# Optimization experiments

Measured on AMD Instinct MI355X. Metric: run time of the kernel, lower is better.

## Reference

```python
import jax, jax.numpy as jnp
import numpy as np
import math

HEAD_DIM = 128
NUM_HEADS = 16
ROPE_BASE = 10000.0


def _rope(x, st_pos):
    # x: [B, S, H, hd], interleaved even/odd rotation as in the torch module
    S, hd = x.shape[1], x.shape[3]
    theta = 1.0 / (ROPE_BASE ** (jnp.arange(0, hd, 2, dtype=jnp.float32) / hd))  # [hd/2]
    pos = jnp.arange(st_pos, st_pos + S, dtype=jnp.float32)[:, None]             # [S,1]
    ang = pos * theta                                                            # [S, hd/2]
    sin = jnp.sin(ang)[None, :, None, :]
    cos = jnp.cos(ang)[None, :, None, :]
    xe, xo = x[..., 0::2], x[..., 1::2]
    re = xe * cos - xo * sin
    ro = xe * sin + xo * cos
    # re-interleave: stack pairs then flatten last two dims
    return jnp.stack([re, ro], axis=-1).reshape(x.shape)


def setup_inputs() -> dict:
    key = jax.random.key(0)
    ks = jax.random.split(key, 6)
    B, S, D = 4, 2048, 2048
    scale = 1.0 / math.sqrt(D)
    x = jax.random.normal(ks[0], (B, S, D), dtype=jnp.float32)
    # causal additive mask (prefill)
    mask = jnp.where(jnp.tril(jnp.ones((S, S), dtype=bool)), 0.0, -1e9).astype(jnp.float32)
    Wq = jax.random.normal(ks[1], (D, NUM_HEADS * HEAD_DIM), dtype=jnp.float32) * scale
    Wk = jax.random.normal(ks[2], (D, NUM_HEADS * HEAD_DIM), dtype=jnp.float32) * scale
    Wv = jax.random.normal(ks[3], (D, NUM_HEADS * HEAD_DIM), dtype=jnp.float32) * scale
    Wo = jax.random.normal(ks[4], (NUM_HEADS * HEAD_DIM, D), dtype=jnp.float32) * scale
    return {"x": x, "mask": mask, "Wq": Wq, "Wk": Wk, "Wv": Wv, "Wo": Wo, "st_pos": 0}


def reference(x, mask, Wq, Wk, Wv, Wo, st_pos):
    B, S, D = x.shape
    H, hd = NUM_HEADS, HEAD_DIM
    q = (x @ Wq).reshape(B, S, H, hd)
    k = (x @ Wk).reshape(B, S, H, hd)
    v = (x @ Wv).reshape(B, S, H, hd)
    q = _rope(q, st_pos)
    k = _rope(k, st_pos)
    # st_pos=0 prefill: cache slice == current k, v; n_rep == 1 (n_kv_heads=num_heads)
    scores = jnp.einsum('bqhd,bkhd->bhqk', q, k) / math.sqrt(hd)
    if mask is not None:
        scores = scores + mask
    attn = jax.nn.softmax(scores, axis=-1)
    a = jnp.einsum('bhqk,bkhd->bqhd', attn, v).reshape(B, S, H * hd)
    return a @ Wo
```

## Files before the change

kernel.cpp:

```cpp
#include <hip/hip_runtime.h>
#include <hip/hip_fp16.h>

typedef _Float16 f16;
typedef __attribute__((ext_vector_type(2))) _Float16 f16x2;
typedef __attribute__((ext_vector_type(4))) _Float16 f16x4v;
typedef __attribute__((ext_vector_type(8))) _Float16 f16x8;
typedef __attribute__((ext_vector_type(4))) float f32x4;
typedef __attribute__((ext_vector_type(4))) int i32x4;

#define DEV __device__ __forceinline__

static constexpr int S_ = 2048;
static constexpr int D_ = 2048;
static constexpr int H_ = 16;
static constexpr int HD_ = 128;
static constexpr int B_ = 4;
static constexpr int QKV_ST = 6144;

typedef const __attribute__((address_space(1))) void* gptr_t;
typedef __attribute__((address_space(3))) void* lptr_t;

DEV void gl_lds16(const void* gsrc, void* lds) {
  __builtin_amdgcn_global_load_lds((gptr_t)gsrc, (lptr_t)lds, 16, 0, 0);
}

DEV int cvt_pk_i32(float a, float b) {
  return __builtin_bit_cast(int, __builtin_amdgcn_cvt_pkrtz(a, b));
}

__global__ __launch_bounds__(256) void cvt_f32_to_f16(const float* __restrict__ in,
                                                      f16* __restrict__ out, long n) {
  long i0 = ((long)blockIdx.x * 256 + threadIdx.x) * 4;
  long stride = (long)gridDim.x * 256 * 4;
  for (long i = i0; i < n; i += stride) {
    float4 v = *(const float4*)(in + i);
    f16x4v o;
    o[0] = (f16)v.x; o[1] = (f16)v.y; o[2] = (f16)v.z; o[3] = (f16)v.w;
    *(f16x4v*)(out + i) = o;
  }
}

__global__ __launch_bounds__(256) void wtrans4(const float* __restrict__ W0, const float* __restrict__ W1,
                                               const float* __restrict__ W2, const float* __restrict__ W3,
                                               f16* __restrict__ Wt) {
  __shared__ float tile[32][33];
  int wi = blockIdx.y;
  const float* W = wi == 0 ? W0 : wi == 1 ? W1 : wi == 2 ? W2 : W3;
  f16* dst = Wt + (size_t)wi * D_ * D_;
  int bx = blockIdx.x & 63, by = blockIdx.x >> 6;
  int r0 = by << 5, c0 = bx << 5;
  int tx = threadIdx.x & 31, ty = threadIdx.x >> 5;
#pragma unroll
  for (int i = 0; i < 4; i++) {
    int r = ty + i * 8;
    tile[r][tx] = W[(size_t)(r0 + r) * D_ + c0 + tx];
  }
  __syncthreads();
#pragma unroll
  for (int i = 0; i < 4; i++) {
    int r = ty + i * 8;
    dst[(size_t)(c0 + r) * D_ + r0 + tx] = (f16)tile[tx][r];
  }
}

DEV f16x8 lds_frag(const f16* half, int row, int s, int lg) {
  int byte = row * 128 + s * 64 + lg * 16;
  byte ^= (row & 4) << 3;
  return *(const f16x8*)((const char*)half + byte);
}

template <typename CT>
__global__ __launch_bounds__(512, 2) void gemm8(const f16* __restrict__ A, const f16* __restrict__ Bt,
                                                CT* __restrict__ C, int M, int N, int K,
                                                int lda, int ldc) {
  __shared__ alignas(16) f16 As[2][2][128 * 64];
  __shared__ alignas(16) f16 Bs[2][2][128 * 64];
  int nbx = N >> 8;
  int nwg = (M >> 8) * nbx;
  int bid = blockIdx.x;
  int wg = (bid & 7) * (nwg >> 3) + (bid >> 3);
  int bx = wg % nbx, by = wg / nbx;
  int tid = threadIdx.x, w = tid >> 6, l = tid & 63;
  int wm = w >> 2, wn = w & 3, lg = l >> 4, ln = l & 15;
  int nt = K >> 6;
  const f16* Ab = A + (size_t)(by * 256) * lda;
  const f16* Bb = Bt + (size_t)(bx * 256) * K;

  auto stageA = [&](const f16* src0, int kt, f16* dst) {
#pragma unroll
    for (int j = 0; j < 2; j++) {
      int c = j * 8 + w;
      int row = c * 8 + (l >> 3);
      int scol = ((l & 7) * 8) ^ ((row & 4) << 2);
      gl_lds16(src0 + (size_t)row * lda + kt * 64 + scol, (char*)dst + c * 1024);
    }
  };
  auto stageB = [&](const f16* src0, int kt, f16* dst) {
#pragma unroll
    for (int j = 0; j < 2; j++) {
      int c = j * 8 + w;
      int row = c * 8 + (l >> 3);
      int scol = ((l & 7) * 8) ^ ((row & 4) << 2);
      gl_lds16(src0 + (size_t)row * K + kt * 64 + scol, (char*)dst + c * 1024);
    }
  };

  f32x4 acc[8][4] = {};

  stageA(Ab, 0, As[0][0]);
  stageA(Ab + (size_t)128 * lda, 0, As[0][1]);
  stageB(Bb, 0, Bs[0][0]);
  stageB(Bb + (size_t)128 * K, 0, Bs[0][1]);
  if (nt > 1) {
    stageB(Bb, 1, Bs[1][0]);
    stageB(Bb + (size_t)128 * K, 1, Bs[1][1]);
  }

  for (int t = 0; t < nt; t++) {
    if (t + 2 < nt) asm volatile("s_waitcnt vmcnt(4)" ::: "memory");
    else            asm volatile("s_waitcnt vmcnt(0)" ::: "memory");
    __builtin_amdgcn_s_barrier();
    asm volatile("" ::: "memory");
    const f16* Ah = As[t & 1][wm];
    const f16* Bh = Bs[t & 1][wn >> 1];
    int br0 = (wn & 1) * 64;
    f16x8 a[4], b0[4], b1[4];
#pragma unroll
    for (int i = 0; i < 4; i++) a[i] = lds_frag(Ah, i * 16 + ln, 0, lg);
#pragma unroll
    for (int i = 0; i < 4; i++) b0[i] = lds_frag(Bh, br0 + i * 16 + ln, 0, lg);
    if (t + 1 < nt) stageA(Ab, t + 1, As[(t + 1) & 1][0]);
    __builtin_amdgcn_s_barrier();
    asm volatile("" ::: "memory");
    __builtin_amdgcn_s_setprio(1);
#pragma unroll
    for (int mi = 0; mi < 4; mi++)
#pragma unroll
      for (int ni = 0; ni < 4; ni++)
        acc[mi][ni] = __builtin_amdgcn_mfma_f32_16x16x32_f16(a[mi], b0[ni], acc[mi][ni], 0, 0, 0);
    __builtin_amdgcn_s_setprio(0);
    __builtin_amdgcn_s_barrier();
    asm volatile("" ::: "memory");
#pragma unroll
    for (int i = 0; i < 4; i++) a[i] = lds_frag(Ah, i * 16 + ln, 1, lg);
#pragma unroll
    for (int i = 0; i < 4; i++) b1[i] = lds_frag(Bh, br0 + i * 16 + ln, 1, lg);
    if (t + 1 < nt) stageA(Ab + (size_t)128 * lda, t + 1, As[(t + 1) & 1][1]);
    __builtin_amdgcn_s_barrier();
    asm volatile("" ::: "memory");
    __builtin_amdgcn_s_setprio(1);
#pragma unroll
    for (int mi = 0; mi < 4; mi++)
#pragma unroll
      for (int ni = 0; ni < 4; ni++)
        acc[mi][ni] = __builtin_amdgcn_mfma_f32_16x16x32_f16(a[mi], b1[ni], acc[mi][ni], 0, 0, 0);
    __builtin_amdgcn_s_setprio(0);
    __builtin_amdgcn_s_barrier();
    asm volatile("" ::: "memory");
#pragma unroll
    for (int i = 0; i < 4; i++) a[i] = lds_frag(Ah, 64 + i * 16 + ln, 0, lg);
    if (t + 2 < nt) stageB(Bb, t + 2, Bs[t & 1][0]);
    __builtin_amdgcn_s_barrier();
    asm volatile("" ::: "memory");
    __builtin_amdgcn_s_setprio(1);
#pragma unroll
    for (int mi = 0; mi < 4; mi++)
#pragma unroll
      for (int ni = 0; ni < 4; ni++)
        acc[mi + 4][ni] = __builtin_amdgcn_mfma_f32_16x16x32_f16(a[mi], b0[ni], acc[mi + 4][ni], 0, 0, 0);
    __builtin_amdgcn_s_setprio(0);
    __builtin_amdgcn_s_barrier();
    asm volatile("" ::: "memory");
#pragma unroll
    for (int i = 0; i < 4; i++) a[i] = lds_frag(Ah, 64 + i * 16 + ln, 1, lg);
    if (t + 2 < nt) stageB(Bb + (size_t)128 * K, t + 2, Bs[t & 1][1]);
    __builtin_amdgcn_s_barrier();
    asm volatile("" ::: "memory");
    __builtin_amdgcn_s_setprio(1);
#pragma unroll
    for (int mi = 0; mi < 4; mi++)
#pragma unroll
      for (int ni = 0; ni < 4; ni++)
        acc[mi + 4][ni] = __builtin_amdgcn_mfma_f32_16x16x32_f16(a[mi], b1[ni], acc[mi + 4][ni], 0, 0, 0);
    __builtin_amdgcn_s_setprio(0);
    __builtin_amdgcn_s_barrier();
    asm volatile("" ::: "memory");
  }

  int row0 = by * 256 + wm * 128;
  int col0 = bx * 256 + wn * 64;
#pragma unroll
  for (int mi = 0; mi < 8; mi++)
#pragma unroll
    for (int ni = 0; ni < 4; ni++)
#pragma unroll
      for (int r4 = 0; r4 < 4; r4++) {
        int row = row0 + mi * 16 + lg * 4 + r4;
        int col = col0 + ni * 16 + ln;
        float o = acc[mi][ni][r4];
        if constexpr (sizeof(CT) == 2) {
          float oo = __shfl_xor(o, 1);
          if (!(ln & 1)) {
            f16x2 pp; pp[0] = (f16)o; pp[1] = (f16)oo;
            *(f16x2*)(&C[(size_t)row * ldc + col]) = pp;
          }
        } else {
          C[(size_t)row * ldc + col] = o;
        }
      }
}

__global__ __launch_bounds__(256) void rope_table(float2* __restrict__ tab, const int* __restrict__ st) {
  int i = blockIdx.x * 256 + threadIdx.x;
  int s = i >> 6, j = i & 63;
  float theta = powf(10000.f, -(float)j / 64.f);
  float ang = (float)(s + st[0]) * theta;
  tab[i] = make_float2(cosf(ang), sinf(ang));
}

__global__ __launch_bounds__(256) void rope_apply_k(f16* __restrict__ QKV, const float2* __restrict__ tab,
                                                    long npairs) {
  long i0 = (long)blockIdx.x * 256 + threadIdx.x;
  long stride = (long)gridDim.x * 256;
  for (long p = i0; p < npairs; p += stride) {
    long row = p >> 10;
    int jp = (int)(p & 1023);
    int s = (int)(row & (S_ - 1));
    float2 cs = tab[s * 64 + (jp & 63)];
    f16* px = QKV + row * QKV_ST + 2048 + 2 * jp;
    f16x2 v = *(const f16x2*)px;
    float xe = (float)v[0], xo = (float)v[1];
    float re = xe * cs.x - xo * cs.y;
    float ro = xe * cs.y + xo * cs.x;
    f16x2 o; o[0] = (f16)re; o[1] = (f16)ro;
    *(f16x2*)px = o;
  }
}

__global__ __launch_bounds__(256) void vtrans2(const f16* __restrict__ QKV, f16* __restrict__ VT2) {
  __shared__ alignas(16) f16 tile[64 * 128];
  int t = blockIdx.x, bh = blockIdx.y, b = bh >> 4, h = bh & 15;
  int tid = threadIdx.x, w = tid >> 6, l = tid & 63, lg = l >> 4, ln = l & 15;
  const f16* src = QKV + (size_t)(b * S_ + t * 64) * QKV_ST + 4096 + h * HD_;
#pragma unroll
  for (int i = 0; i < 4; i++) {
    int idx = i * 256 + tid;
    int r = idx >> 4, c8 = idx & 15;
    int c8s = c8 ^ ((r >> 3) & 3);
    *(f16x8*)(&tile[r * 128 + c8s * 8]) = *(const f16x8*)(src + (size_t)r * QKV_ST + c8 * 8);
  }
  __syncthreads();
  f16* dst = VT2 + (size_t)(bh * 32 + t) * 16 * 512;
#pragma unroll
  for (int ci = 0; ci < 4; ci++) {
    int c = w * 4 + ci;
    int nj = c >> 1, kk = c & 1;
    f16x8 v;
#pragma unroll
    for (int e = 0; e < 8; e++) {
      int r = 16 * (2 * kk + (e >> 2)) + 4 * lg + (e & 3);
      int col = nj * 16 + ln;
      int c8s = (col >> 3) ^ ((r >> 3) & 3);
      v[e] = tile[r * 128 + c8s * 8 + (col & 7)];
    }
    *(f16x8*)(dst + (size_t)c * 512 + l * 8) = v;
  }
}

__global__ __launch_bounds__(512, 4) void attn(f16* __restrict__ QKV, const f16* __restrict__ VT2,
                                               const float2* __restrict__ tab) {
  __shared__ alignas(16) f16 kls[2][2][64 * 128];
  int id = blockIdx.x;
  int r8 = id & 7, j = id >> 3;
  int u = j & 7, g = j >> 3;
  int bh = r8 + (g << 3);
  int b = bh >> 4, h = bh & 15;
  int tid = threadIdx.x, w = tid >> 6, l = tid & 63, lg = l >> 4, ln = l & 15;

  const float QSCALE = 0.12751744910173355f;
  const f16* kp = QKV + (size_t)(b * S_) * QKV_ST + 2048 + h * HD_;
  const f16* vp2 = VT2 + (size_t)bh * 32 * 16 * 512;

  auto stageK = [&](int buf, int half, int kv0) {
#pragma unroll
    for (int jj = 0; jj < 2; jj++) {
      int i = jj * 8 + w;
      int byte = i * 1024 + 16 * l;
      int r = byte >> 8;
      int c = (((byte >> 4) & 15) - r) & 15;
      gl_lds16(kp + (size_t)(kv0 + r) * QKV_ST + c * 8, (char*)kls[buf][half] + i * 1024);
    }
  };

#pragma unroll 1
  for (int pi = 0; pi < 2; pi++) {
    int qsel = pi ? u : 15 - u;
    int q0 = qsel << 7;
    int qrow = q0 + w * 16 + ln;
    f16* qp = QKV + (size_t)(b * S_ + qrow) * QKV_ST + h * HD_;
    const float2* tq = tab + (size_t)qrow * 64;
    f16x8 qf[4];
#pragma unroll
    for (int kc = 0; kc < 4; kc++) {
      f16x8 q = *(const f16x8*)(qp + kc * 32 + lg * 8);
#pragma unroll
      for (int p = 0; p < 4; p++) {
        float2 cs = tq[kc * 16 + lg * 4 + p];
        float e0 = (float)q[2 * p], e1 = (float)q[2 * p + 1];
        q[2 * p] = (f16)((e0 * cs.x - e1 * cs.y) * QSCALE);
        q[2 * p + 1] = (f16)((e0 * cs.y + e1 * cs.x) * QSCALE);
      }
      qf[kc] = q;
    }

    float m = -1e30f, lsum = 0.f;
    f32x4 oacc[8] = {};

    int np = qsel + 1;
    int nt64 = 2 * qsel + 2;
    if (pi) __syncthreads();
    stageK(0, 0, 0);
    stageK(0, 1, 64);
#pragma unroll 1
    for (int p = 0; p < np; p++) {
      __syncthreads();
      if (p + 1 < np) {
        stageK((p + 1) & 1, 0, (2 * p + 2) << 6);
        stageK((p + 1) & 1, 1, (2 * p + 3) << 6);
      }
#pragma unroll 1
      for (int ii = 0; ii < 2; ii++) {
        int t = 2 * p + ii;
        int kv0 = t << 6;
        if (kv0 > q0 + w * 16 + 15) continue;
        const f16* kb = kls[p & 1][ii];
        const f16* vt = vp2 + (size_t)t * 16 * 512;

        f32x4 sf[4];
        __builtin_amdgcn_s_setprio(1);
#pragma unroll
        for (int ni = 0; ni < 4; ni++) {
          int n = ni * 16 + ln;
          f32x4 s = {0.f, 0.f, 0.f, 0.f};
#pragma unroll
          for (int kc = 0; kc < 4; kc++) {
            int mch = kc * 4 + lg;
            f16x8 kf = *(const f16x8*)(&kb[n * 128 + (((mch + n) & 15) << 3)]);
            s = __builtin_amdgcn_mfma_f32_16x16x32_f16(kf, qf[kc], s, 0, 0, 0);
          }
          sf[ni] = s;
        }
        __builtin_amdgcn_s_setprio(0);

        f16x8 vfa[8];
#pragma unroll
        for (int c = 0; c < 8; c++) vfa[c] = *(const f16x8*)(vt + c * 512 + l * 8);

        if (t >= nt64 - 2) {
#pragma unroll
          for (int ni = 0; ni < 4; ni++) {
            int kvg = kv0 + ni * 16 + lg * 4;
#pragma unroll
            for (int r4 = 0; r4 < 4; r4++)
              if (kvg + r4 > qrow) sf[ni][r4] = -1e30f;
          }
        }
        float pm = fmaxf(fmaxf(fmaxf(sf[0][0], sf[0][1]), fmaxf(sf[0][2], sf[0][3])),
                         fmaxf(fmaxf(sf[1][0], sf[1][1]), fmaxf(sf[1][2], sf[1][3])));
        pm = fmaxf(pm, fmaxf(fmaxf(fmaxf(sf[2][0], sf[2][1]), fmaxf(sf[2][2], sf[2][3])),
                             fmaxf(fmaxf(sf[3][0], sf[3][1]), fmaxf(sf[3][2], sf[3][3]))));
        pm = fmaxf(pm, __shfl_xor(pm, 16));
        pm = fmaxf(pm, __shfl_xor(pm, 32));
        float scl = 1.f;
        bool defer = __all(pm <= m + 8.f);
        if (!defer) {
          float mn = fmaxf(m, pm);
          scl = __builtin_amdgcn_exp2f(m - mn);
          m = mn;
        }
        float rsum = 0.f;
#pragma unroll
        for (int ni = 0; ni < 4; ni++)
#pragma unroll
          for (int r4 = 0; r4 < 4; r4++) {
            float pv = __builtin_amdgcn_exp2f(sf[ni][r4] - m);
            sf[ni][r4] = pv;
            rsum += pv;
          }
        lsum = lsum * scl + rsum;

        if (!defer) {
#pragma unroll
          for (int nj = 0; nj < 8; nj++)
#pragma unroll
            for (int r4 = 0; r4 < 4; r4++) oacc[nj][r4] *= scl;
        }

        f16x8 pa[2];
#pragma unroll
        for (int kk = 0; kk < 2; kk++) {
          i32x4 wv;
          wv.x = cvt_pk_i32(sf[2 * kk][0], sf[2 * kk][1]);
          wv.y = cvt_pk_i32(sf[2 * kk][2], sf[2 * kk][3]);
          wv.z = cvt_pk_i32(sf[2 * kk + 1][0], sf[2 * kk + 1][1]);
          wv.w = cvt_pk_i32(sf[2 * kk + 1][2], sf[2 * kk + 1][3]);
          pa[kk] = __builtin_bit_cast(f16x8, wv);
        }

        __builtin_amdgcn_s_setprio(1);
#pragma unroll
        for (int kk = 0; kk < 2; kk++)
#pragma unroll
          for (int nj = 0; nj < 4; nj++)
            oacc[nj] = __builtin_amdgcn_mfma_f32_16x16x32_f16(vfa[nj * 2 + kk], pa[kk], oacc[nj], 0, 0, 0);
#pragma unroll
        for (int njb = 0; njb < 2; njb++) {
          f16x8 vf[4];
#pragma unroll
          for (int jj = 0; jj < 2; jj++)
#pragma unroll
            for (int kk = 0; kk < 2; kk++)
              vf[jj * 2 + kk] = *(const f16x8*)(vt + (size_t)(((4 + njb * 2 + jj) * 2 + kk) * 512) + l * 8);
#pragma unroll
          for (int kk = 0; kk < 2; kk++)
#pragma unroll
            for (int jj = 0; jj < 2; jj++)
              oacc[4 + njb * 2 + jj] = __builtin_amdgcn_mfma_f32_16x16x32_f16(
                  vf[jj * 2 + kk], pa[kk], oacc[4 + njb * 2 + jj], 0, 0, 0);
        }
        __builtin_amdgcn_s_setprio(0);
      }
    }

    lsum += __shfl_xor(lsum, 16);
    lsum += __shfl_xor(lsum, 32);
    float inv = 1.f / lsum;
#pragma unroll
    for (int nj = 0; nj < 8; nj++) {
      f16x4v ov;
#pragma unroll
      for (int r4 = 0; r4 < 4; r4++) ov[r4] = (f16)(oacc[nj][r4] * inv);
      *(f16x4v*)(qp + nj * 16 + lg * 4) = ov;
    }
  }
}

extern "C" void kernel_launch(void* const* d_in, const int* in_sizes, int n_in,
                              void* d_out, int out_size, void* d_ws, size_t ws_size,
                              hipStream_t stream) {
  (void)in_sizes; (void)n_in; (void)out_size; (void)ws_size;
  const float* x = (const float*)d_in[0];
  const float* Wq = (const float*)d_in[2];
  const float* Wk = (const float*)d_in[3];
  const float* Wv = (const float*)d_in[4];
  const float* Wo = (const float*)d_in[5];
  const int* stp = (const int*)d_in[6];
  float* out = (float*)d_out;

  const size_t MS = (size_t)B_ * S_;
  f16* xh = (f16*)d_ws;
  f16* wqt = xh + MS * D_;
  f16* wkt = wqt + (size_t)D_ * D_;
  f16* wvt = wkt + (size_t)D_ * D_;
  f16* wot = wvt + (size_t)D_ * D_;
  f16* qkv = wot + (size_t)D_ * D_;
  float2* tab = (float2*)(qkv + MS * (size_t)QKV_ST);
  f16* vt2 = xh;

  cvt_f32_to_f16<<<16384, 256, 0, stream>>>(x, xh, (long)(MS * D_));
  wtrans4<<<dim3(4096, 4), 256, 0, stream>>>(Wq, Wk, Wv, Wo, wqt);
  gemm8<f16><<<256, 512, 0, stream>>>(xh, wqt, qkv, 8192, 2048, 2048, 2048, QKV_ST);
  gemm8<f16><<<256, 512, 0, stream>>>(xh, wkt, qkv + 2048, 8192, 2048, 2048, 2048, QKV_ST);
  gemm8<f16><<<256, 512, 0, stream>>>(xh, wvt, qkv + 4096, 8192, 2048, 2048, 2048, QKV_ST);
  rope_table<<<512, 256, 0, stream>>>(tab, stp);
  rope_apply_k<<<4096, 256, 0, stream>>>(qkv, tab, (long)(MS * 1024));
  vtrans2<<<dim3(32, 64), 256, 0, stream>>>(qkv, vt2);
  attn<<<512, 512, 0, stream>>>(qkv, vt2, tab);
  gemm8<float><<<256, 512, 0, stream>>>(qkv, wot, out, 8192, 2048, 2048, QKV_ST, 2048);
}
```

Measured before the change: 469.0 us.

## Process two 16-row query groups per wave in attention to reuse K/V fragments

Each wave now handles 32 query rows (two 16-row groups A and B) instead of 16, so every K fragment read from LDS and every V fragment read from global memory feeds two MFMAs. The query tile per block doubles to 256 rows and the grid halves to 256 blocks, with causal pairing adjusted to 8 tiles. This cuts LDS and V-load traffic per FLOP, but it doubles accumulator registers (launch bounds lowered to 2 blocks per SM), reduces parallelism to 256 blocks, and makes causal skipping coarser per wave.

Result: faster. 457.9 us (-2.4%).

```diff
diff --git a/kernel.cpp b/kernel.cpp
--- a/kernel.cpp
+++ b/kernel.cpp
@@ -267,12 +267,12 @@
   }
 }
 
-__global__ __launch_bounds__(512, 4) void attn(f16* __restrict__ QKV, const f16* __restrict__ VT2,
+__global__ __launch_bounds__(512, 2) void attn(f16* __restrict__ QKV, const f16* __restrict__ VT2,
                                                const float2* __restrict__ tab) {
   __shared__ alignas(16) f16 kls[2][2][64 * 128];
   int id = blockIdx.x;
   int r8 = id & 7, j = id >> 3;
-  int u = j & 7, g = j >> 3;
+  int u = j & 3, g = j >> 2;
   int bh = r8 + (g << 3);
   int b = bh >> 4, h = bh & 15;
   int tid = threadIdx.x, w = tid >> 6, l = tid & 63, lg = l >> 4, ln = l & 15;
@@ -294,30 +294,37 @@
 
 #pragma unroll 1
   for (int pi = 0; pi < 2; pi++) {
-    int qsel = pi ? u : 15 - u;
-    int q0 = qsel << 7;
-    int qrow = q0 + w * 16 + ln;
-    f16* qp = QKV + (size_t)(b * S_ + qrow) * QKV_ST + h * HD_;
-    const float2* tq = tab + (size_t)qrow * 64;
-    f16x8 qf[4];
-#pragma unroll
-    for (int kc = 0; kc < 4; kc++) {
-      f16x8 q = *(const f16x8*)(qp + kc * 32 + lg * 8);
-#pragma unroll
-      for (int p = 0; p < 4; p++) {
-        float2 cs = tq[kc * 16 + lg * 4 + p];
-        float e0 = (float)q[2 * p], e1 = (float)q[2 * p + 1];
-        q[2 * p] = (f16)((e0 * cs.x - e1 * cs.y) * QSCALE);
-        q[2 * p + 1] = (f16)((e0 * cs.y + e1 * cs.x) * QSCALE);
+    int qsel = pi ? u : 7 - u;
+    int q0 = qsel << 8;
+    int qrA = q0 + w * 32 + ln;
+    int qrB = qrA + 16;
+    f16* qpA = QKV + (size_t)(b * S_ + qrA) * QKV_ST + h * HD_;
+    f16* qpB = QKV + (size_t)(b * S_ + qrB) * QKV_ST + h * HD_;
+    f16x8 qfA[4], qfB[4];
+#pragma unroll
+    for (int grp = 0; grp < 2; grp++) {
+      f16* qp = grp ? qpB : qpA;
+      const float2* tq = tab + (size_t)(grp ? qrB : qrA) * 64;
+#pragma unroll
+      for (int kc = 0; kc < 4; kc++) {
+        f16x8 q = *(const f16x8*)(qp + kc * 32 + lg * 8);
+#pragma unroll
+        for (int p = 0; p < 4; p++) {
+          float2 cs = tq[kc * 16 + lg * 4 + p];
+          float e0 = (float)q[2 * p], e1 = (float)q[2 * p + 1];
+          q[2 * p] = (f16)((e0 * cs.x - e1 * cs.y) * QSCALE);
+          q[2 * p + 1] = (f16)((e0 * cs.y + e1 * cs.x) * QSCALE);
+        }
+        if (grp) qfB[kc] = q; else qfA[kc] = q;
       }
-      qf[kc] = q;
-    }
-
-    float m = -1e30f, lsum = 0.f;
-    f32x4 oacc[8] = {};
-
-    int np = qsel + 1;
-    int nt64 = 2 * qsel + 2;
+    }
+
+    float mA = -1e30f, lsA = 0.f, mB = -1e30f, lsB = 0.f;
+    f32x4 oaccA[8] = {}, oaccB[8] = {};
+
+    int nt = 4 * qsel + 4;
+    int np = nt >> 1;
+    int twave = (q0 + w * 32 + 31) >> 6;
     if (pi) __syncthreads();
     stageK(0, 0, 0);
     stageK(0, 1, 64);
@@ -332,23 +339,25 @@
       for (int ii = 0; ii < 2; ii++) {
         int t = 2 * p + ii;
         int kv0 = t << 6;
-        if (kv0 > q0 + w * 16 + 15) continue;
+        if (t > twave) continue;
         const f16* kb = kls[p & 1][ii];
         const f16* vt = vp2 + (size_t)t * 16 * 512;
 
-        f32x4 sf[4];
+        f32x4 sfA[4], sfB[4];
         __builtin_amdgcn_s_setprio(1);
 #pragma unroll
         for (int ni = 0; ni < 4; ni++) {
           int n = ni * 16 + ln;
-          f32x4 s = {0.f, 0.f, 0.f, 0.f};
+          f32x4 sA = {0.f, 0.f, 0.f, 0.f};
+          f32x4 sB = {0.f, 0.f, 0.f, 0.f};
 #pragma unroll
           for (int kc = 0; kc < 4; kc++) {
             int mch = kc * 4 + lg;
             f16x8 kf = *(const f16x8*)(&kb[n * 128 + (((mch + n) & 15) << 3)]);
-            s = __builtin_amdgcn_mfma_f32_16x16x32_f16(kf, qf[kc], s, 0, 0, 0);
-          }
-          sf[ni] = s;
+            sA = __builtin_amdgcn_mfma_f32_16x16x32_f16(kf, qfA[kc], sA, 0, 0, 0);
+            sB = __builtin_amdgcn_mfma_f32_16x16x32_f16(kf, qfB[kc], sB, 0, 0, 0);
+          }
+          sfA[ni] = sA; sfB[ni] = sB;
         }
         __builtin_amdgcn_s_setprio(0);
 
@@ -356,63 +365,107 @@
 #pragma unroll
         for (int c = 0; c < 8; c++) vfa[c] = *(const f16x8*)(vt + c * 512 + l * 8);
 
-        if (t >= nt64 - 2) {
+        if (t == twave) {
 #pragma unroll
           for (int ni = 0; ni < 4; ni++) {
             int kvg = kv0 + ni * 16 + lg * 4;
 #pragma unroll
-            for (int r4 = 0; r4 < 4; r4++)
-              if (kvg + r4 > qrow) sf[ni][r4] = -1e30f;
-          }
-        }
-        float pm = fmaxf(fmaxf(fmaxf(sf[0][0], sf[0][1]), fmaxf(sf[0][2], sf[0][3])),
-                         fmaxf(fmaxf(sf[1][0], sf[1][1]), fmaxf(sf[1][2], sf[1][3])));
-        pm = fmaxf(pm, fmaxf(fmaxf(fmaxf(sf[2][0], sf[2][1]), fmaxf(sf[2][2], sf[2][3])),
-                             fmaxf(fmaxf(sf[3][0], sf[3][1]), fmaxf(sf[3][2], sf[3][3]))));
-        pm = fmaxf(pm, __shfl_xor(pm, 16));
-        pm = fmaxf(pm, __shfl_xor(pm, 32));
-        float scl = 1.f;
-        bool defer = __all(pm <= m + 8.f);
-        if (!defer) {
-          float mn = fmaxf(m, pm);
-          scl = __builtin_amdgcn_exp2f(m - mn);
-          m = mn;
-        }
-        float rsum = 0.f;
-#pragma unroll
-        for (int ni = 0; ni < 4; ni++)
-#pragma unroll
-          for (int r4 = 0; r4 < 4; r4++) {
-            float pv = __builtin_amdgcn_exp2f(sf[ni][r4] - m);
-            sf[ni][r4] = pv;
-            rsum += pv;
-          }
-        lsum = lsum * scl + rsum;
-
-        if (!defer) {
-#pragma unroll
-          for (int nj = 0; nj < 8; nj++)
-#pragma unroll
-            for (int r4 = 0; r4 < 4; r4++) oacc[nj][r4] *= scl;
-        }
-
-        f16x8 pa[2];
-#pragma unroll
-        for (int kk = 0; kk < 2; kk++) {
-          i32x4 wv;
-          wv.x = cvt_pk_i32(sf[2 * kk][0], sf[2 * kk][1]);
-          wv.y = cvt_pk_i32(sf[2 * kk][2], sf[2 * kk][3]);
-          wv.z = cvt_pk_i32(sf[2 * kk + 1][0], sf[2 * kk + 1][1]);
-          wv.w = cvt_pk_i32(sf[2 * kk + 1][2], sf[2 * kk + 1][3]);
-          pa[kk] = __builtin_bit_cast(f16x8, wv);
+            for (int r4 = 0; r4 < 4; r4++) {
+              if (kvg + r4 > qrA) sfA[ni][r4] = -1e30f;
+              if (kvg + r4 > qrB) sfB[ni][r4] = -1e30f;
+            }
+          }
+        }
+        f16x8 pa[2], pb[2];
+        {
+          float pm = fmaxf(fmaxf(fmaxf(sfA[0][0], sfA[0][1]), fmaxf(sfA[0][2], sfA[0][3])),
+                           fmaxf(fmaxf(sfA[1][0], sfA[1][1]), fmaxf(sfA[1][2], sfA[1][3])));
+          pm = fmaxf(pm, fmaxf(fmaxf(fmaxf(sfA[2][0], sfA[2][1]), fmaxf(sfA[2][2], sfA[2][3])),
+                               fmaxf(fmaxf(sfA[3][0], sfA[3][1]), fmaxf(sfA[3][2], sfA[3][3]))));
+          pm = fmaxf(pm, __shfl_xor(pm, 16));
+          pm = fmaxf(pm, __shfl_xor(pm, 32));
+          float scl = 1.f;
+          bool defer = __all(pm <= mA + 8.f);
+          if (!defer) {
+            float mn = fmaxf(mA, pm);
+            scl = __builtin_amdgcn_exp2f(mA - mn);
+            mA = mn;
+          }
+          float rsum = 0.f;
+#pragma unroll
+          for (int ni = 0; ni < 4; ni++)
+#pragma unroll
+            for (int r4 = 0; r4 < 4; r4++) {
+              float pv = __builtin_amdgcn_exp2f(sfA[ni][r4] - mA);
+              sfA[ni][r4] = pv;
+              rsum += pv;
+            }
+          lsA = lsA * scl + rsum;
+          if (!defer) {
+#pragma unroll
+            for (int nj = 0; nj < 8; nj++)
+#pragma unroll
+              for (int r4 = 0; r4 < 4; r4++) oaccA[nj][r4] *= scl;
+          }
+#pragma unroll
+          for (int kk = 0; kk < 2; kk++) {
+            i32x4 wv;
+            wv.x = cvt_pk_i32(sfA[2 * kk][0], sfA[2 * kk][1]);
+            wv.y = cvt_pk_i32(sfA[2 * kk][2], sfA[2 * kk][3]);
+            wv.z = cvt_pk_i32(sfA[2 * kk + 1][0], sfA[2 * kk + 1][1]);
+            wv.w = cvt_pk_i32(sfA[2 * kk + 1][2], sfA[2 * kk + 1][3]);
+            pa[kk] = __builtin_bit_cast(f16x8, wv);
+          }
+        }
+        {
+          float pm = fmaxf(fmaxf(fmaxf(sfB[0][0], sfB[0][1]), fmaxf(sfB[0][2], sfB[0][3])),
+                           fmaxf(fmaxf(sfB[1][0], sfB[1][1]), fmaxf(sfB[1][2], sfB[1][3])));
+          pm = fmaxf(pm, fmaxf(fmaxf(fmaxf(sfB[2][0], sfB[2][1]), fmaxf(sfB[2][2], sfB[2][3])),
+                               fmaxf(fmaxf(sfB[3][0], sfB[3][1]), fmaxf(sfB[3][2], sfB[3][3]))));
+          pm = fmaxf(pm, __shfl_xor(pm, 16));
+          pm = fmaxf(pm, __shfl_xor(pm, 32));
+          float scl = 1.f;
+          bool defer = __all(pm <= mB + 8.f);
+          if (!defer) {
+            float mn = fmaxf(mB, pm);
+            scl = __builtin_amdgcn_exp2f(mB - mn);
+            mB = mn;
+          }
+          float rsum = 0.f;
+#pragma unroll
+          for (int ni = 0; ni < 4; ni++)
+#pragma unroll
+            for (int r4 = 0; r4 < 4; r4++) {
+              float pv = __builtin_amdgcn_exp2f(sfB[ni][r4] - mB);
+              sfB[ni][r4] = pv;
+              rsum += pv;
+            }
+          lsB = lsB * scl + rsum;
+          if (!defer) {
+#pragma unroll
+            for (int nj = 0; nj < 8; nj++)
+#pragma unroll
+              for (int r4 = 0; r4 < 4; r4++) oaccB[nj][r4] *= scl;
+          }
+#pragma unroll
+          for (int kk = 0; kk < 2; kk++) {
+            i32x4 wv;
+            wv.x = cvt_pk_i32(sfB[2 * kk][0], sfB[2 * kk][1]);
+            wv.y = cvt_pk_i32(sfB[2 * kk][2], sfB[2 * kk][3]);
+            wv.z = cvt_pk_i32(sfB[2 * kk + 1][0], sfB[2 * kk + 1][1]);
+            wv.w = cvt_pk_i32(sfB[2 * kk + 1][2], sfB[2 * kk + 1][3]);
+            pb[kk] = __builtin_bit_cast(f16x8, wv);
+          }
         }
 
         __builtin_amdgcn_s_setprio(1);
 #pragma unroll
         for (int kk = 0; kk < 2; kk++)
 #pragma unroll
-          for (int nj = 0; nj < 4; nj++)
-            oacc[nj] = __builtin_amdgcn_mfma_f32_16x16x32_f16(vfa[nj * 2 + kk], pa[kk], oacc[nj], 0, 0, 0);
+          for (int nj = 0; nj < 4; nj++) {
+            oaccA[nj] = __builtin_amdgcn_mfma_f32_16x16x32_f16(vfa[nj * 2 + kk], pa[kk], oaccA[nj], 0, 0, 0);
+            oaccB[nj] = __builtin_amdgcn_mfma_f32_16x16x32_f16(vfa[nj * 2 + kk], pb[kk], oaccB[nj], 0, 0, 0);
+          }
 #pragma unroll
         for (int njb = 0; njb < 2; njb++) {
           f16x8 vf[4];
@@ -424,23 +477,31 @@
 #pragma unroll
           for (int kk = 0; kk < 2; kk++)
 #pragma unroll
-            for (int jj = 0; jj < 2; jj++)
-              oacc[4 + njb * 2 + jj] = __builtin_amdgcn_mfma_f32_16x16x32_f16(
-                  vf[jj * 2 + kk], pa[kk], oacc[4 + njb * 2 + jj], 0, 0, 0);
+            for (int jj = 0; jj < 2; jj++) {
+              int nj = 4 + njb * 2 + jj;
+              oaccA[nj] = __builtin_amdgcn_mfma_f32_16x16x32_f16(vf[jj * 2 + kk], pa[kk], oaccA[nj], 0, 0, 0);
+              oaccB[nj] = __builtin_amdgcn_mfma_f32_16x16x32_f16(vf[jj * 2 + kk], pb[kk], oaccB[nj], 0, 0, 0);
+            }
         }
         __builtin_amdgcn_s_setprio(0);
       }
     }
 
-    lsum += __shfl_xor(lsum, 16);
-    lsum += __shfl_xor(lsum, 32);
-    float inv = 1.f / lsum;
+    lsA += __shfl_xor(lsA, 16);
+    lsA += __shfl_xor(lsA, 32);
+    lsB += __shfl_xor(lsB, 16);
+    lsB += __shfl_xor(lsB, 32);
+    float invA = 1.f / lsA, invB = 1.f / lsB;
 #pragma unroll
     for (int nj = 0; nj < 8; nj++) {
-      f16x4v ov;
-#pragma unroll
-      for (int r4 = 0; r4 < 4; r4++) ov[r4] = (f16)(oacc[nj][r4] * inv);
-      *(f16x4v*)(qp + nj * 16 + lg * 4) = ov;
+      f16x4v ovA, ovB;
+#pragma unroll
+      for (int r4 = 0; r4 < 4; r4++) {
+        ovA[r4] = (f16)(oaccA[nj][r4] * invA);
+        ovB[r4] = (f16)(oaccB[nj][r4] * invB);
+      }
+      *(f16x4v*)(qpA + nj * 16 + lg * 4) = ovA;
+      *(f16x4v*)(qpB + nj * 16 + lg * 4) = ovB;
     }
   }
 }
@@ -475,6 +536,6 @@
   rope_table<<<512, 256, 0, stream>>>(tab, stp);
   rope_apply_k<<<4096, 256, 0, stream>>>(qkv, tab, (long)(MS * 1024));
   vtrans2<<<dim3(32, 64), 256, 0, stream>>>(qkv, vt2);
-  attn<<<512, 512, 0, stream>>>(qkv, vt2, tab);
+  attn<<<256, 512, 0, stream>>>(qkv, vt2, tab);
   gemm8<float><<<256, 512, 0, stream>>>(qkv, wot, out, 8192, 2048, 2048, QKV_ST, 2048);
 }
```
